# Kernel tuning notes

Hardware: AMD Instinct MI355X
Metric: run time of the kernel (lower is better)

The kernel has to match this reference:

```python
import jax, jax.numpy as jnp
import numpy as np

D_MODEL = 768; D_STATE = 16; D_CONV = 4; EXPAND = 2
D_INNER = EXPAND * D_MODEL          # 1536
DT_RANK = (D_MODEL + 15) // 16      # 48 (mamba_ssm default dt_rank='auto')
BATCH = 2; SEQ = 2048
LN_EPS = 1e-5


def setup_inputs() -> dict:
    key = jax.random.key(0)
    ks = iter(jax.random.split(key, 64))
    def rn(shape, scale=0.02):
        return jax.random.normal(next(ks), shape, jnp.float32) * scale
    inp = {"x": jax.random.normal(next(ks), (BATCH, SEQ, D_MODEL), jnp.float32)}
    for p in ("f", "b"):
        inp[p + "_in_w"]    = rn((2 * D_INNER, D_MODEL))
        inp[p + "_conv_w"]  = rn((D_INNER, D_CONV), 0.2)
        inp[p + "_conv_b"]  = jnp.zeros((D_INNER,), jnp.float32)
        inp[p + "_xproj_w"] = rn((DT_RANK + 2 * D_STATE, D_INNER))
        inp[p + "_dt_w"]    = rn((D_INNER, DT_RANK), 0.1)
        inp[p + "_dt_b"]    = rn((D_INNER,), 0.1)
        inp[p + "_A_log"]   = jnp.log(jnp.broadcast_to(
            jnp.arange(1, D_STATE + 1, dtype=jnp.float32), (D_INNER, D_STATE)))
        inp[p + "_D"]       = jnp.ones((D_INNER,), jnp.float32)
        inp[p + "_out_w"]   = rn((D_MODEL, D_INNER))
    inp["ln1_g"] = jnp.ones((D_MODEL,), jnp.float32)
    inp["ln1_b"] = jnp.zeros((D_MODEL,), jnp.float32)
    inp["ln2_g"] = jnp.ones((D_MODEL,), jnp.float32)
    inp["ln2_b"] = jnp.zeros((D_MODEL,), jnp.float32)
    inp["ff_w1"] = rn((4 * D_MODEL, D_MODEL))
    inp["ff_b1"] = jnp.zeros((4 * D_MODEL,), jnp.float32)
    inp["ff_w2"] = rn((D_MODEL, 4 * D_MODEL))
    inp["ff_b2"] = jnp.zeros((D_MODEL,), jnp.float32)
    return inp


def _layernorm(x, g, b):
    mu = jnp.mean(x, -1, keepdims=True)
    var = jnp.mean((x - mu) ** 2, -1, keepdims=True)
    return (x - mu) * jax.lax.rsqrt(var + LN_EPS) * g + b


def _selective_scan(u, dt, A, Bm, Cm, Dp):
    # u, dt: [B,L,Dh]; A: [Dh,N]; Bm, Cm: [B,L,N]; Dp: [Dh]
    uT, dtT = jnp.swapaxes(u, 0, 1), jnp.swapaxes(dt, 0, 1)   # time-major
    BmT, CmT = jnp.swapaxes(Bm, 0, 1), jnp.swapaxes(Cm, 0, 1)
    h0 = jnp.zeros((u.shape[0], u.shape[2], A.shape[1]), u.dtype)  # [B,Dh,N]
    def step(h, inp):
        u_t, dt_t, b_t, c_t = inp
        dA = jnp.exp(dt_t[:, :, None] * A)                        # [B,Dh,N]
        h = h * dA + (dt_t * u_t)[:, :, None] * b_t[:, None, :]
        return h, jnp.einsum('bdn,bn->bd', h, c_t)
    _, ys = jax.lax.scan(step, h0, (uT, dtT, BmT, CmT))
    return jnp.swapaxes(ys, 0, 1) + u * Dp


def _mamba(x, in_w, conv_w, conv_b, xproj_w, dt_w, dt_b, A_log, Dp, out_w):
    xz = x @ in_w.T                              # [B,L,2*Dh]
    xh, z = jnp.split(xz, 2, axis=-1)
    # causal depthwise conv over time
    xc = jnp.swapaxes(xh, 1, 2)                  # [B,Dh,L]
    xc = jnp.pad(xc, ((0, 0), (0, 0), (D_CONV - 1, 0)))
    xc = jax.lax.conv_general_dilated(xc, conv_w[:, None, :], (1,), 'VALID',
                                      feature_group_count=D_INNER)
    xh = jax.nn.silu(jnp.swapaxes(xc + conv_b[None, :, None], 1, 2))
    x_dbl = xh @ xproj_w.T                       # [B,L,dt_rank+2N]
    dt, Bm, Cm = jnp.split(x_dbl, [DT_RANK, DT_RANK + D_STATE], axis=-1)
    dt = jax.nn.softplus(dt @ dt_w.T + dt_b)     # [B,L,Dh]
    A = -jnp.exp(A_log)                          # [Dh,N]
    y = _selective_scan(xh, dt, A, Bm, Cm, Dp)
    return (y * jax.nn.silu(z)) @ out_w.T


def _forward(x, f_in_w, f_conv_w, f_conv_b, f_xproj_w, f_dt_w, f_dt_b, f_A_log,
             f_D, f_out_w, b_in_w, b_conv_w, b_conv_b, b_xproj_w, b_dt_w, b_dt_b,
             b_A_log, b_D, b_out_w, ln1_g, ln1_b, ln2_g, ln2_b,
             ff_w1, ff_b1, ff_w2, ff_b2):
    xn = _layernorm(x, ln1_g, ln1_b)
    fo = _mamba(xn, f_in_w, f_conv_w, f_conv_b, f_xproj_w, f_dt_w, f_dt_b,
                f_A_log, f_D, f_out_w)
    bo = _mamba(xn[:, ::-1], b_in_w, b_conv_w, b_conv_b, b_xproj_w, b_dt_w,
                b_dt_b, b_A_log, b_D, b_out_w)[:, ::-1]
    m = _layernorm(fo + bo, ln2_g, ln2_b)
    ff = jax.nn.gelu(m @ ff_w1.T + ff_b1, approximate=False) @ ff_w2.T + ff_b2
    return ff + x


def reference(x, f_in_w, f_conv_w, f_conv_b, f_xproj_w, f_dt_w, f_dt_b, f_A_log,
              f_D, f_out_w, b_in_w, b_conv_w, b_conv_b, b_xproj_w, b_dt_w, b_dt_b,
              b_A_log, b_D, b_out_w, ln1_g, ln1_b, ln2_g, ln2_b,
              ff_w1, ff_b1, ff_w2, ff_b2):
    return _forward(x, f_in_w, f_conv_w, f_conv_b, f_xproj_w, f_dt_w, f_dt_b,
                    f_A_log, f_D, f_out_w, b_in_w, b_conv_w, b_conv_b, b_xproj_w,
                    b_dt_w, b_dt_b, b_A_log, b_D, b_out_w, ln1_g, ln1_b, ln2_g,
                    ln2_b, ff_w1, ff_b1, ff_w2, ff_b2)
```

## Files before the change

kernel.cpp:

```cpp
#include <hip/hip_runtime.h>
#include <cstdint>
#include <cstddef>

#define BATCH_ 2
#define SEQ_ 2048
#define DM 768
#define DH 1536
#define NS 16
#define RK 48
#define MR (BATCH_*SEQ_)
#define NCH 32
#define CL (SEQ_/NCH)
#define NCHAN (2*BATCH_*DH)
#define NDBLK (DH/256)

typedef __attribute__((ext_vector_type(8))) short short8b;
typedef __attribute__((ext_vector_type(4))) float f32x4;
typedef __attribute__((address_space(1))) const unsigned int gas_u32;
typedef __attribute__((address_space(3))) unsigned int las_u32;

__device__ __forceinline__ float sigmoidf_(float x){ return 1.f/(1.f+__expf(-x)); }

__device__ __forceinline__ void split1(float x, ushort& h, ushort& l){
  unsigned u = __float_as_uint(x);
  h = (ushort)(u >> 16);
  float lf = x - __uint_as_float(u & 0xFFFF0000u);
  l = (ushort)(__float_as_uint(lf) >> 16);
}

__global__ __launch_bounds__(256) void split_kernel(const float* __restrict__ in,
    ushort* __restrict__ hi, ushort* __restrict__ lo, int n4)
{
  int i = blockIdx.x*256 + threadIdx.x;
  if (i >= n4) return;
  float4 v = ((const float4*)in)[i];
  ushort h0,h1,h2,h3,l0,l1,l2,l3;
  split1(v.x,h0,l0); split1(v.y,h1,l1); split1(v.z,h2,l2); split1(v.w,h3,l3);
  ((ushort4*)hi)[i] = make_ushort4(h0,h1,h2,h3);
  ((ushort4*)lo)[i] = make_ushort4(l0,l1,l2,l3);
}

__global__ __launch_bounds__(256) void ln1_kernel(const float* __restrict__ x,
    const float* __restrict__ g, const float* __restrict__ bta,
    ushort* __restrict__ xnh, ushort* __restrict__ xnl)
{
  int row = blockIdx.x;
  int tid = threadIdx.x;
  __shared__ float s1[256], s2[256];
  float v[3]; float sum=0.f, sq=0.f;
  const float* xr = x + (size_t)row*DM;
  #pragma unroll
  for (int i=0;i<3;i++){ v[i] = xr[tid + i*256]; sum += v[i]; sq += v[i]*v[i]; }
  s1[tid]=sum; s2[tid]=sq; __syncthreads();
  for (int off=128; off>0; off>>=1){
    if (tid<off){ s1[tid]+=s1[tid+off]; s2[tid]+=s2[tid+off]; }
    __syncthreads();
  }
  float mean = s1[0] * (1.f/DM);
  float var  = s2[0] * (1.f/DM) - mean*mean;
  float rstd = rsqrtf(var + 1e-5f);
  #pragma unroll
  for (int i=0;i<3;i++){
    int c = tid + i*256;
    float val = (v[i]-mean)*rstd*g[c] + bta[c];
    ushort h, lo_;
    split1(val, h, lo_);
    xnh[(size_t)row*DM + c] = h;  xnl[(size_t)row*DM + c] = lo_;
  }
}

__global__ __launch_bounds__(256) void ln2_kernel(const float* __restrict__ fo,
    const float* __restrict__ bo, const float* __restrict__ g,
    const float* __restrict__ bta, ushort* __restrict__ mh, ushort* __restrict__ ml)
{
  int row = blockIdx.x;
  int tid = threadIdx.x;
  int bb = row >> 11, l = row & (SEQ_-1);
  __shared__ float s1[256], s2[256];
  size_t rrow = ((size_t)bb*SEQ_ + (SEQ_-1-l))*DM;
  float v[3]; float sum=0.f, sq=0.f;
  #pragma unroll
  for (int i=0;i<3;i++){
    int c = tid + i*256;
    v[i] = fo[(size_t)row*DM + c] + bo[rrow + c];
    sum += v[i]; sq += v[i]*v[i];
  }
  s1[tid]=sum; s2[tid]=sq; __syncthreads();
  for (int off=128; off>0; off>>=1){
    if (tid<off){ s1[tid]+=s1[tid+off]; s2[tid]+=s2[tid+off]; }
    __syncthreads();
  }
  float mean = s1[0] * (1.f/DM);
  float var  = s2[0] * (1.f/DM) - mean*mean;
  float rstd = rsqrtf(var + 1e-5f);
  #pragma unroll
  for (int i=0;i<3;i++){
    int c = tid + i*256;
    float val = (v[i]-mean)*rstd*g[c] + bta[c];
    ushort h, lo_;
    split1(val, h, lo_);
    mh[(size_t)row*DM + c] = h;  ml[(size_t)row*DM + c] = lo_;
  }
}

template<int ACT, bool RAW>
__global__ __launch_bounds__(256) void gemm_nt(const float* __restrict__ A, int lda,
    const float* __restrict__ W, const float* __restrict__ bias,
    float* __restrict__ C, int ldc, const float* __restrict__ res,
    int M, int N, int K, int Kc)
{
  __shared__ float As[16][64];
  __shared__ float Ws[16][64];
  int tid = threadIdx.x;
  int tx = tid & 15, ty = tid >> 4;
  int m0 = blockIdx.y * 64, n0 = blockIdx.x * 64;
  int lm = tid >> 2;
  int lk = (tid & 3) * 4;
  const int kbeg = RAW ? blockIdx.z*Kc : 0;
  const int kend = RAW ? kbeg + Kc : K;
  float acc[4][4] = {};
  for (int k0 = kbeg; k0 < kend; k0 += 16) {
    float4 av = *(const float4*)(A + (size_t)(m0+lm)*lda + k0 + lk);
    As[lk+0][lm] = av.x; As[lk+1][lm] = av.y; As[lk+2][lm] = av.z; As[lk+3][lm] = av.w;
    int wn = n0 + lm;
    float4 wv = make_float4(0.f,0.f,0.f,0.f);
    if (wn < N) wv = *(const float4*)(W + (size_t)wn*K + k0 + lk);
    Ws[lk+0][lm] = wv.x; Ws[lk+1][lm] = wv.y; Ws[lk+2][lm] = wv.z; Ws[lk+3][lm] = wv.w;
    __syncthreads();
    #pragma unroll
    for (int k = 0; k < 16; ++k) {
      float4 a = *(const float4*)&As[k][ty*4];
      float4 w = *(const float4*)&Ws[k][tx*4];
      acc[0][0] += a.x*w.x; acc[0][1] += a.x*w.y; acc[0][2] += a.x*w.z; acc[0][3] += a.x*w.w;
      acc[1][0] += a.y*w.x; acc[1][1] += a.y*w.y; acc[1][2] += a.y*w.z; acc[1][3] += a.y*w.w;
      acc[2][0] += a.z*w.x; acc[2][1] += a.z*w.y; acc[2][2] += a.z*w.z; acc[2][3] += a.z*w.w;
      acc[3][0] += a.w*w.x; acc[3][1] += a.w*w.y; acc[3][2] += a.w*w.z; acc[3][3] += a.w*w.w;
    }
    __syncthreads();
  }
  if constexpr (RAW){
    float* P = C + (size_t)blockIdx.z*((size_t)M*N);
    #pragma unroll
    for (int i=0;i<4;i++){
      int row = m0 + ty*4 + i;
      #pragma unroll
      for (int j=0;j<4;j++){
        int col = n0 + tx*4 + j;
        if (col < N) P[(size_t)row*N + col] = acc[i][j];
      }
    }
  } else {
    #pragma unroll
    for (int i=0;i<4;i++){
      int row = m0 + ty*4 + i;
      #pragma unroll
      for (int j=0;j<4;j++){
        int col = n0 + tx*4 + j;
        if (col < N) {
          float vv = acc[i][j];
          if (bias) vv += bias[col];
          if (ACT == 1) vv = (vv > 20.f) ? vv : log1pf(expf(vv));
          if (res) vv += res[(size_t)row*ldc + col];
          C[(size_t)row*ldc + col] = vv;
        }
      }
    }
  }
}

template<int ACT, int OUT>
__global__ __launch_bounds__(256,2) void gemm_mfma(
    const ushort* __restrict__ Ah_g, const ushort* __restrict__ Al_g, int ldaA,
    const ushort* __restrict__ Wh_g, const ushort* __restrict__ Wl_g,
    const ushort* __restrict__ Wh2, const ushort* __restrict__ Wl2,
    float* __restrict__ C2,
    const float* __restrict__ bias, float* __restrict__ C,
    ushort* __restrict__ Oh, ushort* __restrict__ Ol,
    int ldc, const float* __restrict__ res,
    int M, int N, int K, int Kc)
{
  __shared__ short8b L[2][2048];
  const int tid = threadIdx.x;
  const int m0 = blockIdx.y*128, n0 = blockIdx.x*128;
  const int lane = tid & 63, wv = tid >> 6;
  const int wr = (wv>>1)*64, wc = (wv&1)*64;
  const int li = lane & 15, lg = lane >> 4;
  const int z = blockIdx.z;
  const int kbeg = (OUT==1) ? z*Kc : 0;
  const int nkt = ((OUT==1) ? Kc : K) >> 5;

  const ushort* WhS = Wh_g; const ushort* WlS = Wl_g;
  float* Cd = C;
  int revmask = 0;
  if constexpr (OUT==3){
    if (z==1){ WhS = Wh2; WlS = Wl2; Cd = C2; revmask = SEQ_-1; }
  }

  const int lr8 = lane >> 3, ls = lane & 7;
  const int sl = ls ^ lr8;
  const int chunk = (sl & 3) * 8;
  const ushort* gA = (sl < 4) ? Ah_g : Al_g;
  const ushort* gB = (sl < 4) ? WhS : WlS;
  const ushort* aAddr[4]; const ushort* bAddr[4];
  #pragma unroll
  for (int i=0;i<4;i++){
    int rg = (m0 + wv*32 + i*8 + lr8) ^ revmask;
    aAddr[i] = gA + (size_t)rg*ldaA + kbeg + chunk;
    int rb = n0 + wv*32 + i*8 + lr8;
    bAddr[i] = gB + (size_t)rb*K + kbeg + chunk;
  }

  f32x4 acc[4][4];
  #pragma unroll
  for (int i=0;i<4;i++)
    #pragma unroll
    for (int j=0;j<4;j++) acc[i][j] = (f32x4){0.f,0.f,0.f,0.f};

  #define STAGE_(kt_, b_) { \
    const int ko_ = (kt_)*32; \
    _Pragma("unroll") \
    for (int i=0;i<4;i++){ \
      __builtin_amdgcn_global_load_lds((gas_u32*)(aAddr[i]+ko_), \
          (las_u32*)&L[b_][(wv*32+i*8)*8], 16, 0, 0); \
      __builtin_amdgcn_global_load_lds((gas_u32*)(bAddr[i]+ko_), \
          (las_u32*)&L[b_][1024+(wv*32+i*8)*8], 16, 0, 0); \
    } }

  STAGE_(0, 0);
  __syncthreads();

  for (int kt=0; kt<nkt; ++kt){
    const int cur = kt & 1;
    if (kt+1 < nkt) STAGE_(kt+1, cur^1);
    short8b afh[4],afl[4],bfh[4],bfl[4];
    #pragma unroll
    for (int f=0; f<4; f++){
      int sa = (wr+f*16+li)*8 + (lg ^ (li&7));
      int sb = 1024 + (wc+f*16+li)*8 + (lg ^ (li&7));
      afh[f]=L[cur][sa]; afl[f]=L[cur][sa^4];
      bfh[f]=L[cur][sb]; bfl[f]=L[cur][sb^4];
    }
    #pragma unroll
    for (int fr=0;fr<4;fr++)
      #pragma unroll
      for (int fc=0;fc<4;fc++){
        acc[fr][fc]=__builtin_amdgcn_mfma_f32_16x16x32_bf16(afh[fr],bfh[fc],acc[fr][fc],0,0,0);
        acc[fr][fc]=__builtin_amdgcn_mfma_f32_16x16x32_bf16(afh[fr],bfl[fc],acc[fr][fc],0,0,0);
        acc[fr][fc]=__builtin_amdgcn_mfma_f32_16x16x32_bf16(afl[fr],bfh[fc],acc[fr][fc],0,0,0);
      }
    __syncthreads();
  }
  #undef STAGE_

  if constexpr (OUT==1){
    float* P = C + (size_t)z*((size_t)M*N);
    #pragma unroll
    for (int fr=0;fr<4;fr++)
      #pragma unroll
      for (int fc=0;fc<4;fc++){
        int col = n0 + wc + fc*16 + li;
        int row = m0 + wr + fr*16 + lg*4;
        #pragma unroll
        for (int rg=0;rg<4;rg++)
          P[(size_t)(row+rg)*N + col] = acc[fr][fc][rg];
      }
  } else if constexpr (OUT==2){
    #pragma unroll
    for (int fr=0;fr<4;fr++)
      #pragma unroll
      for (int fc=0;fc<4;fc++){
        int col = n0 + wc + fc*16 + li;
        int row = m0 + wr + fr*16 + lg*4;
        float bv = bias ? bias[col] : 0.f;
        #pragma unroll
        for (int rg=0;rg<4;rg++){
          float t = acc[fr][fc][rg] + bv;
          t = 0.5f*t*(1.f+erff(t*0.70710678118654752f));
          ushort h, lo_;
          split1(t, h, lo_);
          Oh[(size_t)(row+rg)*ldc + col] = h;
          Ol[(size_t)(row+rg)*ldc + col] = lo_;
        }
      }
  } else {
    #pragma unroll
    for (int fr=0;fr<4;fr++)
      #pragma unroll
      for (int fc=0;fc<4;fc++){
        int col = n0 + wc + fc*16 + li;
        int row = m0 + wr + fr*16 + lg*4;
        float bv = bias ? bias[col] : 0.f;
        #pragma unroll
        for (int rg=0;rg<4;rg++){
          float t = acc[fr][fc][rg] + bv;
          if (res) t += res[(size_t)(row+rg)*ldc + col];
          Cd[(size_t)(row+rg)*ldc + col] = t;
        }
      }
  }
}

__global__ __launch_bounds__(256) void reduce_split(const float* __restrict__ P,
    const float* __restrict__ bias, const float* __restrict__ res,
    float* __restrict__ C, int N, size_t elems, int nsplit)
{
  size_t i = ((size_t)blockIdx.x*256 + threadIdx.x)*4;
  float4 s = *(const float4*)(P + i);
  for (int k=1;k<nsplit;k++){
    float4 p = *(const float4*)(P + (size_t)k*elems + i);
    s.x+=p.x; s.y+=p.y; s.z+=p.z; s.w+=p.w;
  }
  if (bias){
    int col = (int)(i % (size_t)N);
    const float4 b = *(const float4*)(bias + col);
    s.x+=b.x; s.y+=b.y; s.z+=b.z; s.w+=b.w;
  }
  if (res){
    const float4 r = *(const float4*)(res + i);
    s.x+=r.x; s.y+=r.y; s.z+=r.z; s.w+=r.w;
  }
  *(float4*)(C + i) = s;
}

__global__ __launch_bounds__(256) void conv_silu_kernel(const float* __restrict__ xz,
    const float* __restrict__ cw, const float* __restrict__ cb, float* __restrict__ xh)
{
  int idx = blockIdx.x*256 + threadIdx.x;
  int d = idx % DH;
  int row = idx / DH;
  int l = row & (SEQ_-1);
  const float* base = xz + (size_t)row*(2*DH) + d;
  float acc = cb[d];
  #pragma unroll
  for (int j=0;j<4;j++){
    int ll = l - 3 + j;
    if (ll >= 0) acc += cw[d*4+j] * base[(ptrdiff_t)(j-3)*(2*DH)];
  }
  xh[(size_t)row*DH + d] = acc * sigmoidf_(acc);
}

__global__ __launch_bounds__(256) void scan_p1_kernel(
    const float* __restrict__ dt0, const float* __restrict__ xh0, const float* __restrict__ xd0,
    const float* __restrict__ Al0,
    const float* __restrict__ dt1, const float* __restrict__ xh1, const float* __restrict__ xd1,
    const float* __restrict__ Al1,
    float* __restrict__ hend, float* __restrict__ dtsum)
{
  int tid = threadIdx.x;
  int bid = blockIdx.x;
  int dblk = bid % NDBLK;
  int t   = bid / NDBLK;
  int c   = t & (NCH-1);
  int db  = t >> 5;
  int dir = db >> 1, bb = db & 1;
  int d = dblk*256 + tid;
  const float* dt = dir ? dt1 : dt0;
  const float* xh = dir ? xh1 : xh0;
  const float* xd = dir ? xd1 : xd0;
  const float* Al = dir ? Al1 : Al0;

  __shared__ float sB[CL][NS];
  {
    const float* xdb = xd + ((size_t)bb*SEQ_ + (size_t)c*CL)*80 + RK;
    int row = tid >> 2, part = tid & 3;
    *(float4*)&sB[row][part*4] = *(const float4*)(xdb + (size_t)row*80 + part*4);
  }
  float An[NS];
  {
    const float4* ap = (const float4*)(Al + (size_t)d*NS);
    #pragma unroll
    for (int q=0;q<4;q++){
      float4 a = ap[q];
      An[4*q+0] = -__expf(a.x); An[4*q+1] = -__expf(a.y);
      An[4*q+2] = -__expf(a.z); An[4*q+3] = -__expf(a.w);
    }
  }
  __syncthreads();

  float h[NS];
  #pragma unroll
  for (int n=0;n<NS;n++) h[n] = 0.f;
  float dts = 0.f;
  size_t base = ((size_t)bb*SEQ_ + (size_t)c*CL)*DH + d;
  #pragma unroll 4
  for (int l=0;l<CL;++l){
    float dtv = dt[base], uv = xh[base];
    float du = dtv*uv;
    float Bv[NS];
    *(float4*)&Bv[0]  = *(const float4*)&sB[l][0];
    *(float4*)&Bv[4]  = *(const float4*)&sB[l][4];
    *(float4*)&Bv[8]  = *(const float4*)&sB[l][8];
    *(float4*)&Bv[12] = *(const float4*)&sB[l][12];
    #pragma unroll
    for (int n=0;n<NS;n++)
      h[n] = h[n]*__expf(dtv*An[n]) + du*Bv[n];
    dts += dtv;
    base += DH;
  }
  size_t unit = ((size_t)db*DH + d)*NCH + c;
  float4* hp = (float4*)(hend + unit*NS);
  hp[0] = make_float4(h[0],h[1],h[2],h[3]);
  hp[1] = make_float4(h[4],h[5],h[6],h[7]);
  hp[2] = make_float4(h[8],h[9],h[10],h[11]);
  hp[3] = make_float4(h[12],h[13],h[14],h[15]);
  dtsum[(size_t)c*NCHAN + (size_t)db*DH + d] = dts;
}

__global__ __launch_bounds__(256) void scan_p2_kernel(
    const float* __restrict__ Al0, const float* __restrict__ Al1,
    float* __restrict__ hend, const float* __restrict__ dtsum)
{
  int t = blockIdx.x*256 + threadIdx.x;
  int n = t & 15;
  int ch = t >> 4;
  int d  = ch % DH;
  int dir = (ch / DH) >> 1;
  const float* Al = dir ? Al1 : Al0;
  float An = -__expf(Al[d*NS + n]);
  float h0 = 0.f;
  size_t ub = (size_t)ch * NCH;
  #pragma unroll
  for (int c = 0; c < NCH; ++c) {
    float P  = __expf(An * dtsum[(size_t)c*NCHAN + ch]);
    float he = hend[(ub + c)*NS + n];
    hend[(ub + c)*NS + n] = h0;
    h0 = h0 * P + he;
  }
}

__global__ __launch_bounds__(256) void scan_p3_kernel(
    const float* __restrict__ dt0, const float* __restrict__ xh0, const float* __restrict__ xd0,
    const float* __restrict__ z0, const float* __restrict__ Al0, const float* __restrict__ Dp0,
    ushort* __restrict__ yg0,
    const float* __restrict__ dt1, const float* __restrict__ xh1, const float* __restrict__ xd1,
    const float* __restrict__ z1, const float* __restrict__ Al1, const float* __restrict__ Dp1,
    ushort* __restrict__ yg1,
    const float* __restrict__ hstart)
{
  int tid = threadIdx.x;
  int bid = blockIdx.x;
  int dblk = bid % NDBLK;
  int t   = bid / NDBLK;
  int c   = t & (NCH-1);
  int db  = t >> 5;
  int dir = db >> 1, bb = db & 1;
  int d = dblk*256 + tid;
  const float* dt = dir ? dt1 : dt0;
  const float* xh = dir ? xh1 : xh0;
  const float* xd = dir ? xd1 : xd0;
  const float* zp = dir ? z1  : z0;
  const float* Al = dir ? Al1 : Al0;
  const float* Dp = dir ? Dp1 : Dp0;
  ushort*      yg = dir ? yg1 : yg0;

  __shared__ float sBC[CL][2*NS];
  {
    const float* xdb = xd + ((size_t)bb*SEQ_ + (size_t)c*CL)*80 + RK;
    #pragma unroll
    for (int i=0;i<2;i++){
      int idx = tid + i*256;
      int row = idx >> 3, part = idx & 7;
      *(float4*)&sBC[row][part*4] = *(const float4*)(xdb + (size_t)row*80 + part*4);
    }
  }
  float An[NS];
  {
    const float4* ap = (const float4*)(Al + (size_t)d*NS);
    #pragma unroll
    for (int q=0;q<4;q++){
      float4 a = ap[q];
      An[4*q+0] = -__expf(a.x); An[4*q+1] = -__expf(a.y);
      An[4*q+2] = -__expf(a.z); An[4*q+3] = -__expf(a.w);
    }
  }
  float Dd = Dp[d];
  __syncthreads();

  size_t unit = ((size_t)db*DH + d)*NCH + c;
  float h[NS];
  {
    const float4* hp = (const float4*)(hstart + unit*NS);
    float4 h0=hp[0], h1=hp[1], h2=hp[2], h3=hp[3];
    h[0]=h0.x; h[1]=h0.y; h[2]=h0.z; h[3]=h0.w;
    h[4]=h1.x; h[5]=h1.y; h[6]=h1.z; h[7]=h1.w;
    h[8]=h2.x; h[9]=h2.y; h[10]=h2.z; h[11]=h2.w;
    h[12]=h3.x; h[13]=h3.y; h[14]=h3.z; h[15]=h3.w;
  }
  size_t base = ((size_t)bb*SEQ_ + (size_t)c*CL)*DH + d;
  size_t zidx = ((size_t)bb*SEQ_ + (size_t)c*CL)*(size_t)(2*DH) + DH + d;
  size_t yrow = ((size_t)bb*SEQ_ + (size_t)c*CL)*(size_t)(4*DH) + d;
  #pragma unroll 2
  for (int l=0;l<CL;++l){
    float dtv = dt[base], uv = xh[base];
    float zv = zp[zidx];
    float du = dtv*uv;
    float Bv[NS], Cv[NS];
    *(float4*)&Bv[0]  = *(const float4*)&sBC[l][0];
    *(float4*)&Bv[4]  = *(const float4*)&sBC[l][4];
    *(float4*)&Bv[8]  = *(const float4*)&sBC[l][8];
    *(float4*)&Bv[12] = *(const float4*)&sBC[l][12];
    *(float4*)&Cv[0]  = *(const float4*)&sBC[l][16];
    *(float4*)&Cv[4]  = *(const float4*)&sBC[l][20];
    *(float4*)&Cv[8]  = *(const float4*)&sBC[l][24];
    *(float4*)&Cv[12] = *(const float4*)&sBC[l][28];
    float y = 0.f;
    #pragma unroll
    for (int n=0;n<NS;n++){
      h[n] = h[n]*__expf(dtv*An[n]) + du*Bv[n];
      y = fmaf(h[n], Cv[n], y);
    }
    float yv = (y + uv*Dd) * (zv * sigmoidf_(zv));
    ushort hh, ll;
    split1(yv, hh, ll);
    yg[yrow] = hh; yg[yrow + DH] = ll;
    base += DH; zidx += 2*DH; yrow += 4*DH;
  }
}

template<int ACT>
static inline void launch_gemm(const float* A, int lda, const float* W, const float* bias,
                               float* C, int ldc, const float* res,
                               int M, int N, int K, hipStream_t s)
{
  dim3 grid((N+63)/64, M/64);
  gemm_nt<ACT,false><<<grid, dim3(256), 0, s>>>(A, lda, W, bias, C, ldc, res, M, N, K, 0);
}

static inline void launch_gemm_splitk(const float* A, int lda, const float* W,
                                      float* P, int M, int N, int K, int nsplit,
                                      hipStream_t s)
{
  dim3 grid((N+63)/64, M/64, nsplit);
  gemm_nt<0,true><<<grid, dim3(256), 0, s>>>(A, lda, W, nullptr, P, N, nullptr,
                                             M, N, K, K/nsplit);
}

extern "C" void kernel_launch(void* const* d_in, const int* in_sizes, int n_in,
                              void* d_out, int out_size, void* d_ws, size_t ws_size,
                              hipStream_t stream)
{
  const float* x        = (const float*)d_in[0];
  const float* f_in_w   = (const float*)d_in[1];
  const float* f_conv_w = (const float*)d_in[2];
  const float* f_conv_b = (const float*)d_in[3];
  const float* f_xproj  = (const float*)d_in[4];
  const float* f_dt_w   = (const float*)d_in[5];
  const float* f_dt_b   = (const float*)d_in[6];
  const float* f_A_log  = (const float*)d_in[7];
  const float* f_D      = (const float*)d_in[8];
  const float* f_out_w  = (const float*)d_in[9];
  const float* b_in_w   = (const float*)d_in[10];
  const float* b_conv_w = (const float*)d_in[11];
  const float* b_conv_b = (const float*)d_in[12];
  const float* b_xproj  = (const float*)d_in[13];
  const float* b_dt_w   = (const float*)d_in[14];
  const float* b_dt_b   = (const float*)d_in[15];
  const float* b_A_log  = (const float*)d_in[16];
  const float* b_D      = (const float*)d_in[17];
  const float* b_out_w  = (const float*)d_in[18];
  const float* ln1_g    = (const float*)d_in[19];
  const float* ln1_b    = (const float*)d_in[20];
  const float* ln2_g    = (const float*)d_in[21];
  const float* ln2_b    = (const float*)d_in[22];
  const float* ff_w1    = (const float*)d_in[23];
  const float* ff_b1    = (const float*)d_in[24];
  const float* ff_w2    = (const float*)d_in[25];
  const float* ff_b2    = (const float*)d_in[26];
  float* out = (float*)d_out;

  float* ws = (float*)d_ws;
  size_t o = 0;
  float* xz_f   = ws + o; o += (size_t)MR*2*DH;
  float* xz_b   = ws + o; o += (size_t)MR*2*DH;
  float* xh_f   = ws + o; o += (size_t)MR*DH;
  float* xh_b   = ws + o; o += (size_t)MR*DH;
  float* xdbl_f = ws + o; o += (size_t)MR*80;
  float* xdbl_b = ws + o; o += (size_t)MR*80;
  float* dtb_f  = ws + o; o += (size_t)MR*DH;
  float* dtb_b  = ws + o; o += (size_t)MR*DH;
  float* xnbf   = ws + o; o += (size_t)MR*DM;
  float* dtsum  = ws + o; o += (size_t)NCHAN*NCH;
  float* wbf    = ws + o; o += (size_t)2*(2*DH*DM);

  ushort* xnh = (ushort*)xnbf;
  ushort* xnl = xnh + (size_t)MR*DM;
  ushort* yg_f = (ushort*)xz_f;
  ushort* yg_b = (ushort*)xz_b;
  ushort* wreg = (ushort*)wbf;
  ushort* f_inh = wreg;                       ushort* f_inl = wreg + (size_t)2*DH*DM;
  ushort* b_inh = wreg + (size_t)2*(2*DH*DM); ushort* b_inl = wreg + (size_t)3*(2*DH*DM);
  ushort* f_oth = wreg;                       ushort* f_otl = wreg + (size_t)DM*DH;
  ushort* b_oth = wreg + (size_t)2*DM*DH;     ushort* b_otl = wreg + (size_t)3*DM*DH;
  ushort* w1h   = wreg;                       ushort* w1l   = wreg + (size_t)4*DM*DM;
  ushort* w2h   = wreg + (size_t)2*(4*DM*DM); ushort* w2l   = wreg + (size_t)3*(4*DM*DM);
  float* hend  = xnbf;
  float* partX = xnbf;
  ushort* mh   = (ushort*)xh_f;
  ushort* ml   = mh + (size_t)MR*DM;
  float* fo    = xh_b;
  float* bo    = xh_b + (size_t)MR*DM;
  float* part1 = dtb_f;
  ushort* ffhh = (ushort*)dtb_f;
  ushort* ffhl = ffhh + (size_t)MR*4*DM;
  float* part2 = xz_b;
  const size_t EL = (size_t)MR*DM;
  const size_t EL2 = (size_t)MR*80;

  split_kernel<<<(2*DH*DM/4+255)/256, 256, 0, stream>>>(f_in_w, f_inh, f_inl, 2*DH*DM/4);
  split_kernel<<<(2*DH*DM/4+255)/256, 256, 0, stream>>>(b_in_w, b_inh, b_inl, 2*DH*DM/4);
  ln1_kernel<<<MR, 256, 0, stream>>>(x, ln1_g, ln1_b, xnh, xnl);
  {
    dim3 grid((2*DH)/128, MR/128, 2);
    gemm_mfma<0,3><<<grid, dim3(256), 0, stream>>>(xnh, xnl, DM, f_inh, f_inl,
        b_inh, b_inl, xz_b, nullptr, xz_f, nullptr, nullptr, 2*DH, nullptr,
        MR, 2*DH, DM, 0);
  }
  split_kernel<<<(DM*DH/4+255)/256, 256, 0, stream>>>(f_out_w, f_oth, f_otl, DM*DH/4);
  split_kernel<<<(DM*DH/4+255)/256, 256, 0, stream>>>(b_out_w, b_oth, b_otl, DM*DH/4);
  conv_silu_kernel<<<(MR*DH)/256, 256, 0, stream>>>(xz_f, f_conv_w, f_conv_b, xh_f);
  conv_silu_kernel<<<(MR*DH)/256, 256, 0, stream>>>(xz_b, b_conv_w, b_conv_b, xh_b);
  launch_gemm_splitk(xh_f, DH, f_xproj, partX, MR, 80, DH, 8, stream);
  reduce_split<<<(int)(EL2/1024), 256, 0, stream>>>(partX, nullptr, nullptr, xdbl_f, 80, EL2, 8);
  launch_gemm_splitk(xh_b, DH, b_xproj, partX, MR, 80, DH, 8, stream);
  reduce_split<<<(int)(EL2/1024), 256, 0, stream>>>(partX, nullptr, nullptr, xdbl_b, 80, EL2, 8);
  launch_gemm<1>(xdbl_f, 80, f_dt_w, f_dt_b, dtb_f, DH, nullptr, MR, DH, RK, stream);
  launch_gemm<1>(xdbl_b, 80, b_dt_w, b_dt_b, dtb_b, DH, nullptr, MR, DH, RK, stream);
  scan_p1_kernel<<<4*NCH*NDBLK, 256, 0, stream>>>(
      dtb_f, xh_f, xdbl_f, f_A_log,
      dtb_b, xh_b, xdbl_b, b_A_log,
      hend, dtsum);
  scan_p2_kernel<<<(NCHAN*NS)/256, 256, 0, stream>>>(f_A_log, b_A_log, hend, dtsum);
  scan_p3_kernel<<<4*NCH*NDBLK, 256, 0, stream>>>(
      dtb_f, xh_f, xdbl_f, xz_f, f_A_log, f_D, yg_f,
      dtb_b, xh_b, xdbl_b, xz_b, b_A_log, b_D, yg_b,
      hend);
  {
    dim3 grid(DM/128, MR/128, 4);
    gemm_mfma<0,1><<<grid, dim3(256), 0, stream>>>(yg_f, yg_f + DH, 4*DH,
        f_oth, f_otl, nullptr, nullptr, nullptr, nullptr, part1, nullptr, nullptr,
        DM, nullptr, MR, DM, DH, DH/4);
    reduce_split<<<(int)(EL/1024), 256, 0, stream>>>(part1, nullptr, nullptr, fo, DM, EL, 4);
    gemm_mfma<0,1><<<grid, dim3(256), 0, stream>>>(yg_b, yg_b + DH, 4*DH,
        b_oth, b_otl, nullptr, nullptr, nullptr, nullptr, part1, nullptr, nullptr,
        DM, nullptr, MR, DM, DH, DH/4);
    reduce_split<<<(int)(EL/1024), 256, 0, stream>>>(part1, nullptr, nullptr, bo, DM, EL, 4);
  }
  split_kernel<<<(4*DM*DM/4+255)/256, 256, 0, stream>>>(ff_w1, w1h, w1l, 4*DM*DM/4);
  split_kernel<<<(4*DM*DM/4+255)/256, 256, 0, stream>>>(ff_w2, w2h, w2l, 4*DM*DM/4);
  ln2_kernel<<<MR, 256, 0, stream>>>(fo, bo, ln2_g, ln2_b, mh, ml);
  {
    dim3 grid1((4*DM)/128, MR/128);
    gemm_mfma<2,2><<<grid1, dim3(256), 0, stream>>>(mh, ml, DM, w1h, w1l,
        nullptr, nullptr, nullptr, ff_b1, nullptr, ffhh, ffhl, 4*DM, nullptr,
        MR, 4*DM, DM, 0);
    dim3 grid2(DM/128, MR/128, 4);
    gemm_mfma<0,1><<<grid2, dim3(256), 0, stream>>>(ffhh, ffhl, 4*DM, w2h, w2l,
        nullptr, nullptr, nullptr, nullptr, part2, nullptr, nullptr,
        DM, nullptr, MR, DM, 4*DM, (4*DM)/4);
    reduce_split<<<(int)(EL/1024), 256, 0, stream>>>(part2, ff_b2, x, out, DM, EL, 4);
  }
}
```

Measured before the change: 779.0 us.

## Move x_proj and dt_proj GEMMs to split-bf16 MFMA path with padded weights

```diff
diff --git a/kernel.cpp b/kernel.cpp
--- a/kernel.cpp
+++ b/kernel.cpp
@@ -8,6 +8,8 @@
 #define DH 1536
 #define NS 16
 #define RK 48
+#define XDW 128
+#define KDT 64
 #define MR (BATCH_*SEQ_)
 #define NCH 32
 #define CL (SEQ_/NCH)
@@ -26,6 +28,9 @@
   h = (ushort)(u >> 16);
   float lf = x - __uint_as_float(u & 0xFFFF0000u);
   l = (ushort)(__float_as_uint(lf) >> 16);
+}
+__device__ __forceinline__ float joinhl(ushort h, ushort l){
+  return __uint_as_float((unsigned)h<<16) + __uint_as_float((unsigned)l<<16);
 }
 
 __global__ __launch_bounds__(256) void split_kernel(const float* __restrict__ in,
@@ -40,6 +45,19 @@
   ((ushort4*)lo)[i] = make_ushort4(l0,l1,l2,l3);
 }
 
+__global__ __launch_bounds__(256) void padsplit_kernel(const float* __restrict__ in,
+    ushort* __restrict__ hi, ushort* __restrict__ lo,
+    int rin, int cin, int rout, int cout)
+{
+  int i = blockIdx.x*256 + threadIdx.x;
+  if (i >= rout*cout) return;
+  int r = i / cout, c = i % cout;
+  float v = (r < rin && c < cin) ? in[(size_t)r*cin + c] : 0.f;
+  ushort h, l;
+  split1(v, h, l);
+  hi[i] = h; lo[i] = l;
+}
+
 __global__ __launch_bounds__(256) void ln1_kernel(const float* __restrict__ x,
     const float* __restrict__ g, const float* __restrict__ bta,
     ushort* __restrict__ xnh, ushort* __restrict__ xnl)
@@ -100,71 +118,6 @@
     ushort h, lo_;
     split1(val, h, lo_);
     mh[(size_t)row*DM + c] = h;  ml[(size_t)row*DM + c] = lo_;
-  }
-}
-
-template<int ACT, bool RAW>
-__global__ __launch_bounds__(256) void gemm_nt(const float* __restrict__ A, int lda,
-    const float* __restrict__ W, const float* __restrict__ bias,
-    float* __restrict__ C, int ldc, const float* __restrict__ res,
-    int M, int N, int K, int Kc)
-{
-  __shared__ float As[16][64];
-  __shared__ float Ws[16][64];
-  int tid = threadIdx.x;
-  int tx = tid & 15, ty = tid >> 4;
-  int m0 = blockIdx.y * 64, n0 = blockIdx.x * 64;
-  int lm = tid >> 2;
-  int lk = (tid & 3) * 4;
-  const int kbeg = RAW ? blockIdx.z*Kc : 0;
-  const int kend = RAW ? kbeg + Kc : K;
-  float acc[4][4] = {};
-  for (int k0 = kbeg; k0 < kend; k0 += 16) {
-    float4 av = *(const float4*)(A + (size_t)(m0+lm)*lda + k0 + lk);
-    As[lk+0][lm] = av.x; As[lk+1][lm] = av.y; As[lk+2][lm] = av.z; As[lk+3][lm] = av.w;
-    int wn = n0 + lm;
-    float4 wv = make_float4(0.f,0.f,0.f,0.f);
-    if (wn < N) wv = *(const float4*)(W + (size_t)wn*K + k0 + lk);
-    Ws[lk+0][lm] = wv.x; Ws[lk+1][lm] = wv.y; Ws[lk+2][lm] = wv.z; Ws[lk+3][lm] = wv.w;
-    __syncthreads();
-    #pragma unroll
-    for (int k = 0; k < 16; ++k) {
-      float4 a = *(const float4*)&As[k][ty*4];
-      float4 w = *(const float4*)&Ws[k][tx*4];
-      acc[0][0] += a.x*w.x; acc[0][1] += a.x*w.y; acc[0][2] += a.x*w.z; acc[0][3] += a.x*w.w;
-      acc[1][0] += a.y*w.x; acc[1][1] += a.y*w.y; acc[1][2] += a.y*w.z; acc[1][3] += a.y*w.w;
-      acc[2][0] += a.z*w.x; acc[2][1] += a.z*w.y; acc[2][2] += a.z*w.z; acc[2][3] += a.z*w.w;
-      acc[3][0] += a.w*w.x; acc[3][1] += a.w*w.y; acc[3][2] += a.w*w.z; acc[3][3] += a.w*w.w;
-    }
-    __syncthreads();
-  }
-  if constexpr (RAW){
-    float* P = C + (size_t)blockIdx.z*((size_t)M*N);
-    #pragma unroll
-    for (int i=0;i<4;i++){
-      int row = m0 + ty*4 + i;
-      #pragma unroll
-      for (int j=0;j<4;j++){
-        int col = n0 + tx*4 + j;
-        if (col < N) P[(size_t)row*N + col] = acc[i][j];
-      }
-    }
-  } else {
-    #pragma unroll
-    for (int i=0;i<4;i++){
-      int row = m0 + ty*4 + i;
-      #pragma unroll
-      for (int j=0;j<4;j++){
-        int col = n0 + tx*4 + j;
-        if (col < N) {
-          float vv = acc[i][j];
-          if (bias) vv += bias[col];
-          if (ACT == 1) vv = (vv > 20.f) ? vv : log1pf(expf(vv));
-          if (res) vv += res[(size_t)row*ldc + col];
-          C[(size_t)row*ldc + col] = vv;
-        }
-      }
-    }
   }
 }
 
@@ -181,11 +134,22 @@
 {
   __shared__ short8b L[2][2048];
   const int tid = threadIdx.x;
-  const int m0 = blockIdx.y*128, n0 = blockIdx.x*128;
+  int bx = blockIdx.x, by = blockIdx.y, bz = blockIdx.z;
+  {
+    const int Gx = gridDim.x, Gy = gridDim.y;
+    const int n = Gx*Gy*gridDim.z;
+    if ((n & 7) == 0){
+      int lid = bx + Gx*(by + Gy*bz);
+      int lid2 = (lid & 7)*(n >> 3) + (lid >> 3);
+      bx = lid2 % Gx; lid2 /= Gx;
+      by = lid2 % Gy; bz = lid2 / Gy;
+    }
+  }
+  const int m0 = by*128, n0 = bx*128;
   const int lane = tid & 63, wv = tid >> 6;
   const int wr = (wv>>1)*64, wc = (wv&1)*64;
   const int li = lane & 15, lg = lane >> 4;
-  const int z = blockIdx.z;
+  const int z = bz;
   const int kbeg = (OUT==1) ? z*Kc : 0;
   const int nkt = ((OUT==1) ? Kc : K) >> 5;
 
@@ -293,6 +257,7 @@
         #pragma unroll
         for (int rg=0;rg<4;rg++){
           float t = acc[fr][fc][rg] + bv;
+          if constexpr (ACT==1) t = (t > 20.f) ? t : log1pf(expf(t));
           if (res) t += res[(size_t)(row+rg)*ldc + col];
           Cd[(size_t)(row+rg)*ldc + col] = t;
         }
@@ -322,8 +287,35 @@
   *(float4*)(C + i) = s;
 }
 
+__global__ __launch_bounds__(256) void reduce_xproj(const float* __restrict__ P,
+    float* __restrict__ xdbl, ushort* __restrict__ aH, ushort* __restrict__ aL,
+    size_t elems, int nsplit)
+{
+  size_t i = ((size_t)blockIdx.x*256 + threadIdx.x)*4;
+  float4 s = *(const float4*)(P + i);
+  for (int k=1;k<nsplit;k++){
+    float4 p = *(const float4*)(P + (size_t)k*elems + i);
+    s.x+=p.x; s.y+=p.y; s.z+=p.z; s.w+=p.w;
+  }
+  *(float4*)(xdbl + i) = s;
+  int col = (int)(i & (XDW-1));
+  if (col < KDT){
+    size_t row = i >> 7;
+    float vs[4] = {s.x, s.y, s.z, s.w};
+    ushort h[4], l[4];
+    #pragma unroll
+    for (int j=0;j<4;j++){
+      float v = (col + j < RK) ? vs[j] : 0.f;
+      split1(v, h[j], l[j]);
+    }
+    *(ushort4*)(aH + row*KDT + col) = make_ushort4(h[0],h[1],h[2],h[3]);
+    *(ushort4*)(aL + row*KDT + col) = make_ushort4(l[0],l[1],l[2],l[3]);
+  }
+}
+
 __global__ __launch_bounds__(256) void conv_silu_kernel(const float* __restrict__ xz,
-    const float* __restrict__ cw, const float* __restrict__ cb, float* __restrict__ xh)
+    const float* __restrict__ cw, const float* __restrict__ cb,
+    ushort* __restrict__ xhh, ushort* __restrict__ xhl)
 {
   int idx = blockIdx.x*256 + threadIdx.x;
   int d = idx % DH;
@@ -336,13 +328,18 @@
     int ll = l - 3 + j;
     if (ll >= 0) acc += cw[d*4+j] * base[(ptrdiff_t)(j-3)*(2*DH)];
   }
-  xh[(size_t)row*DH + d] = acc * sigmoidf_(acc);
+  float v = acc * sigmoidf_(acc);
+  ushort h, lo_;
+  split1(v, h, lo_);
+  xhh[idx] = h; xhl[idx] = lo_;
 }
 
 __global__ __launch_bounds__(256) void scan_p1_kernel(
-    const float* __restrict__ dt0, const float* __restrict__ xh0, const float* __restrict__ xd0,
+    const float* __restrict__ dt0, const ushort* __restrict__ xhh0,
+    const ushort* __restrict__ xhl0, const float* __restrict__ xd0,
     const float* __restrict__ Al0,
-    const float* __restrict__ dt1, const float* __restrict__ xh1, const float* __restrict__ xd1,
+    const float* __restrict__ dt1, const ushort* __restrict__ xhh1,
+    const ushort* __restrict__ xhl1, const float* __restrict__ xd1,
     const float* __restrict__ Al1,
     float* __restrict__ hend, float* __restrict__ dtsum)
 {
@@ -355,15 +352,16 @@
   int dir = db >> 1, bb = db & 1;
   int d = dblk*256 + tid;
   const float* dt = dir ? dt1 : dt0;
-  const float* xh = dir ? xh1 : xh0;
+  const ushort* xhh = dir ? xhh1 : xhh0;
+  const ushort* xhl = dir ? xhl1 : xhl0;
   const float* xd = dir ? xd1 : xd0;
   const float* Al = dir ? Al1 : Al0;
 
   __shared__ float sB[CL][NS];
   {
-    const float* xdb = xd + ((size_t)bb*SEQ_ + (size_t)c*CL)*80 + RK;
+    const float* xdb = xd + ((size_t)bb*SEQ_ + (size_t)c*CL)*XDW + RK;
     int row = tid >> 2, part = tid & 3;
-    *(float4*)&sB[row][part*4] = *(const float4*)(xdb + (size_t)row*80 + part*4);
+    *(float4*)&sB[row][part*4] = *(const float4*)(xdb + (size_t)row*XDW + part*4);
   }
   float An[NS];
   {
@@ -384,7 +382,8 @@
   size_t base = ((size_t)bb*SEQ_ + (size_t)c*CL)*DH + d;
   #pragma unroll 4
   for (int l=0;l<CL;++l){
-    float dtv = dt[base], uv = xh[base];
+    float dtv = dt[base];
+    float uv = joinhl(xhh[base], xhl[base]);
     float du = dtv*uv;
     float Bv[NS];
     *(float4*)&Bv[0]  = *(const float4*)&sB[l][0];
@@ -429,12 +428,14 @@
 }
 
 __global__ __launch_bounds__(256) void scan_p3_kernel(
-    const float* __restrict__ dt0, const float* __restrict__ xh0, const float* __restrict__ xd0,
-    const float* __restrict__ z0, const float* __restrict__ Al0, const float* __restrict__ Dp0,
-    ushort* __restrict__ yg0,
-    const float* __restrict__ dt1, const float* __restrict__ xh1, const float* __restrict__ xd1,
-    const float* __restrict__ z1, const float* __restrict__ Al1, const float* __restrict__ Dp1,
-    ushort* __restrict__ yg1,
+    const float* __restrict__ dt0, const ushort* __restrict__ xhh0,
+    const ushort* __restrict__ xhl0, const float* __restrict__ xd0,
+    const float* __restrict__ z0, const float* __restrict__ Al0,
+    const float* __restrict__ Dp0, ushort* __restrict__ yg0,
+    const float* __restrict__ dt1, const ushort* __restrict__ xhh1,
+    const ushort* __restrict__ xhl1, const float* __restrict__ xd1,
+    const float* __restrict__ z1, const float* __restrict__ Al1,
+    const float* __restrict__ Dp1, ushort* __restrict__ yg1,
     const float* __restrict__ hstart)
 {
   int tid = threadIdx.x;
@@ -446,7 +447,8 @@
   int dir = db >> 1, bb = db & 1;
   int d = dblk*256 + tid;
   const float* dt = dir ? dt1 : dt0;
-  const float* xh = dir ? xh1 : xh0;
+  const ushort* xhh = dir ? xhh1 : xhh0;
+  const ushort* xhl = dir ? xhl1 : xhl0;
   const float* xd = dir ? xd1 : xd0;
   const float* zp = dir ? z1  : z0;
   const float* Al = dir ? Al1 : Al0;
@@ -455,12 +457,12 @@
 
   __shared__ float sBC[CL][2*NS];
   {
-    const float* xdb = xd + ((size_t)bb*SEQ_ + (size_t)c*CL)*80 + RK;
+    const float* xdb = xd + ((size_t)bb*SEQ_ + (size_t)c*CL)*XDW + RK;
     #pragma unroll
     for (int i=0;i<2;i++){
       int idx = tid + i*256;
       int row = idx >> 3, part = idx & 7;
-      *(float4*)&sBC[row][part*4] = *(const float4*)(xdb + (size_t)row*80 + part*4);
+      *(float4*)&sBC[row][part*4] = *(const float4*)(xdb + (size_t)row*XDW + part*4);
     }
   }
   float An[NS];
@@ -491,7 +493,8 @@
   size_t yrow = ((size_t)bb*SEQ_ + (size_t)c*CL)*(size_t)(4*DH) + d;
   #pragma unroll 2
   for (int l=0;l<CL;++l){
-    float dtv = dt[base], uv = xh[base];
+    float dtv = dt[base];
+    float uv = joinhl(xhh[base], xhl[base]);
     float zv = zp[zidx];
     float du = dtv*uv;
     float Bv[NS], Cv[NS];
@@ -515,24 +518,6 @@
     yg[yrow] = hh; yg[yrow + DH] = ll;
     base += DH; zidx += 2*DH; yrow += 4*DH;
   }
-}
-
-template<int ACT>
-static inline void launch_gemm(const float* A, int lda, const float* W, const float* bias,
-                               float* C, int ldc, const float* res,
-                               int M, int N, int K, hipStream_t s)
-{
-  dim3 grid((N+63)/64, M/64);
-  gemm_nt<ACT,false><<<grid, dim3(256), 0, s>>>(A, lda, W, bias, C, ldc, res, M, N, K, 0);
-}
-
-static inline void launch_gemm_splitk(const float* A, int lda, const float* W,
-                                      float* P, int M, int N, int K, int nsplit,
-                                      hipStream_t s)
-{
-  dim3 grid((N+63)/64, M/64, nsplit);
-  gemm_nt<0,true><<<grid, dim3(256), 0, s>>>(A, lda, W, nullptr, P, N, nullptr,
-                                             M, N, K, K/nsplit);
 }
 
 extern "C" void kernel_launch(void* const* d_in, const int* in_sizes, int n_in,
@@ -574,16 +559,23 @@
   float* xz_b   = ws + o; o += (size_t)MR*2*DH;
   float* xh_f   = ws + o; o += (size_t)MR*DH;
   float* xh_b   = ws + o; o += (size_t)MR*DH;
-  float* xdbl_f = ws + o; o += (size_t)MR*80;
-  float* xdbl_b = ws + o; o += (size_t)MR*80;
+  float* xdbl_f = ws + o; o += (size_t)MR*XDW;
+  float* xdbl_b = ws + o; o += (size_t)MR*XDW;
   float* dtb_f  = ws + o; o += (size_t)MR*DH;
   float* dtb_b  = ws + o; o += (size_t)MR*DH;
+  float* dthA_f = ws + o; o += (size_t)MR*KDT;
+  float* dthA_b = ws + o; o += (size_t)MR*KDT;
   float* xnbf   = ws + o; o += (size_t)MR*DM;
   float* dtsum  = ws + o; o += (size_t)NCHAN*NCH;
   float* wbf    = ws + o; o += (size_t)2*(2*DH*DM);
+  float* wsm    = ws + o; o += (size_t)2*128*DH + (size_t)2*DH*KDT;
 
   ushort* xnh = (ushort*)xnbf;
   ushort* xnl = xnh + (size_t)MR*DM;
+  ushort* xhh_f = (ushort*)xh_f;  ushort* xhl_f = xhh_f + (size_t)MR*DH;
+  ushort* xhh_b = (ushort*)xh_b;  ushort* xhl_b = xhh_b + (size_t)MR*DH;
+  ushort* aHf = (ushort*)dthA_f;  ushort* aLf = aHf + (size_t)MR*KDT;
+  ushort* aHb = (ushort*)dthA_b;  ushort* aLb = aHb + (size_t)MR*KDT;
   ushort* yg_f = (ushort*)xz_f;
   ushort* yg_b = (ushort*)xz_b;
   ushort* wreg = (ushort*)wbf;
@@ -593,8 +585,13 @@
   ushort* b_oth = wreg + (size_t)2*DM*DH;     ushort* b_otl = wreg + (size_t)3*DM*DH;
   ushort* w1h   = wreg;                       ushort* w1l   = wreg + (size_t)4*DM*DM;
   ushort* w2h   = wreg + (size_t)2*(4*DM*DM); ushort* w2l   = wreg + (size_t)3*(4*DM*DM);
+  ushort* wsu = (ushort*)wsm;
+  ushort* xpwh_f = wsu;                         ushort* xpwl_f = xpwh_f + (size_t)128*DH;
+  ushort* xpwh_b = xpwl_f + (size_t)128*DH;     ushort* xpwl_b = xpwh_b + (size_t)128*DH;
+  ushort* dtwh_f = xpwl_b + (size_t)128*DH;     ushort* dtwl_f = dtwh_f + (size_t)DH*KDT;
+  ushort* dtwh_b = dtwl_f + (size_t)DH*KDT;     ushort* dtwl_b = dtwh_b + (size_t)DH*KDT;
   float* hend  = xnbf;
-  float* partX = xnbf;
+  float* partX = dtb_f;
   ushort* mh   = (ushort*)xh_f;
   ushort* ml   = mh + (size_t)MR*DM;
   float* fo    = xh_b;
@@ -603,11 +600,15 @@
   ushort* ffhh = (ushort*)dtb_f;
   ushort* ffhl = ffhh + (size_t)MR*4*DM;
   float* part2 = xz_b;
-  const size_t EL = (size_t)MR*DM;
-  const size_t EL2 = (size_t)MR*80;
+  const size_t EL  = (size_t)MR*DM;
+  const size_t ELX = (size_t)MR*XDW;
 
   split_kernel<<<(2*DH*DM/4+255)/256, 256, 0, stream>>>(f_in_w, f_inh, f_inl, 2*DH*DM/4);
   split_kernel<<<(2*DH*DM/4+255)/256, 256, 0, stream>>>(b_in_w, b_inh, b_inl, 2*DH*DM/4);
+  padsplit_kernel<<<(128*DH+255)/256, 256, 0, stream>>>(f_xproj, xpwh_f, xpwl_f, 80, DH, 128, DH);
+  padsplit_kernel<<<(128*DH+255)/256, 256, 0, stream>>>(b_xproj, xpwh_b, xpwl_b, 80, DH, 128, DH);
+  padsplit_kernel<<<(DH*KDT+255)/256, 256, 0, stream>>>(f_dt_w, dtwh_f, dtwl_f, DH, RK, DH, KDT);
+  padsplit_kernel<<<(DH*KDT+255)/256, 256, 0, stream>>>(b_dt_w, dtwh_b, dtwl_b, DH, RK, DH, KDT);
   ln1_kernel<<<MR, 256, 0, stream>>>(x, ln1_g, ln1_b, xnh, xnl);
   {
     dim3 grid((2*DH)/128, MR/128, 2);
@@ -617,22 +618,36 @@
   }
   split_kernel<<<(DM*DH/4+255)/256, 256, 0, stream>>>(f_out_w, f_oth, f_otl, DM*DH/4);
   split_kernel<<<(DM*DH/4+255)/256, 256, 0, stream>>>(b_out_w, b_oth, b_otl, DM*DH/4);
-  conv_silu_kernel<<<(MR*DH)/256, 256, 0, stream>>>(xz_f, f_conv_w, f_conv_b, xh_f);
-  conv_silu_kernel<<<(MR*DH)/256, 256, 0, stream>>>(xz_b, b_conv_w, b_conv_b, xh_b);
-  launch_gemm_splitk(xh_f, DH, f_xproj, partX, MR, 80, DH, 8, stream);
-  reduce_split<<<(int)(EL2/1024), 256, 0, stream>>>(partX, nullptr, nullptr, xdbl_f, 80, EL2, 8);
-  launch_gemm_splitk(xh_b, DH, b_xproj, partX, MR, 80, DH, 8, stream);
-  reduce_split<<<(int)(EL2/1024), 256, 0, stream>>>(partX, nullptr, nullptr, xdbl_b, 80, EL2, 8);
-  launch_gemm<1>(xdbl_f, 80, f_dt_w, f_dt_b, dtb_f, DH, nullptr, MR, DH, RK, stream);
-  launch_gemm<1>(xdbl_b, 80, b_dt_w, b_dt_b, dtb_b, DH, nullptr, MR, DH, RK, stream);
+  conv_silu_kernel<<<(MR*DH)/256, 256, 0, stream>>>(xz_f, f_conv_w, f_conv_b, xhh_f, xhl_f);
+  conv_silu_kernel<<<(MR*DH)/256, 256, 0, stream>>>(xz_b, b_conv_w, b_conv_b, xhh_b, xhl_b);
+  {
+    dim3 grid(1, MR/128, 8);
+    gemm_mfma<0,1><<<grid, dim3(256), 0, stream>>>(xhh_f, xhl_f, DH, xpwh_f, xpwl_f,
+        nullptr, nullptr, nullptr, nullptr, partX, nullptr, nullptr,
+        XDW, nullptr, MR, XDW, DH, DH/8);
+    reduce_xproj<<<(int)(ELX/1024), 256, 0, stream>>>(partX, xdbl_f, aHf, aLf, ELX, 8);
+    gemm_mfma<0,1><<<grid, dim3(256), 0, stream>>>(xhh_b, xhl_b, DH, xpwh_b, xpwl_b,
+        nullptr, nullptr, nullptr, nullptr, partX, nullptr, nullptr,
+        XDW, nullptr, MR, XDW, DH, DH/8);
+    reduce_xproj<<<(int)(ELX/1024), 256, 0, stream>>>(partX, xdbl_b, aHb, aLb, ELX, 8);
+  }
+  {
+    dim3 grid(DH/128, MR/128, 1);
+    gemm_mfma<1,0><<<grid, dim3(256), 0, stream>>>(aHf, aLf, KDT, dtwh_f, dtwl_f,
+        nullptr, nullptr, nullptr, f_dt_b, dtb_f, nullptr, nullptr,
+        DH, nullptr, MR, DH, KDT, 0);
+    gemm_mfma<1,0><<<grid, dim3(256), 0, stream>>>(aHb, aLb, KDT, dtwh_b, dtwl_b,
+        nullptr, nullptr, nullptr, b_dt_b, dtb_b, nullptr, nullptr,
+        DH, nullptr, MR, DH, KDT, 0);
+  }
   scan_p1_kernel<<<4*NCH*NDBLK, 256, 0, stream>>>(
-      dtb_f, xh_f, xdbl_f, f_A_log,
-      dtb_b, xh_b, xdbl_b, b_A_log,
+      dtb_f, xhh_f, xhl_f, xdbl_f, f_A_log,
+      dtb_b, xhh_b, xhl_b, xdbl_b, b_A_log,
       hend, dtsum);
   scan_p2_kernel<<<(NCHAN*NS)/256, 256, 0, stream>>>(f_A_log, b_A_log, hend, dtsum);
   scan_p3_kernel<<<4*NCH*NDBLK, 256, 0, stream>>>(
-      dtb_f, xh_f, xdbl_f, xz_f, f_A_log, f_D, yg_f,
-      dtb_b, xh_b, xdbl_b, xz_b, b_A_log, b_D, yg_b,
+      dtb_f, xhh_f, xhl_f, xdbl_f, xz_f, f_A_log, f_D, yg_f,
+      dtb_b, xhh_b, xhl_b, xdbl_b, xz_b, b_A_log, b_D, yg_b,
       hend);
   {
     dim3 grid(DM/128, MR/128, 4);
@@ -649,7 +664,7 @@
   split_kernel<<<(4*DM*DM/4+255)/256, 256, 0, stream>>>(ff_w2, w2h, w2l, 4*DM*DM/4);
   ln2_kernel<<<MR, 256, 0, stream>>>(fo, bo, ln2_g, ln2_b, mh, ml);
   {
-    dim3 grid1((4*DM)/128, MR/128);
+    dim3 grid1((4*DM)/128, MR/128, 1);
     gemm_mfma<2,2><<<grid1, dim3(256), 0, stream>>>(mh, ml, DM, w1h, w1l,
         nullptr, nullptr, nullptr, ff_b1, nullptr, ffhh, ffhl, 4*DM, nullptr,
         MR, 4*DM, DM, 0);
```

After: 873.6 us. +12.1%, slower.

## Add single-buffer GEMM variant and XCD-aware block remapping

Applied to the files above, without the earlier changes.

```diff
diff --git a/kernel.cpp b/kernel.cpp
--- a/kernel.cpp
+++ b/kernel.cpp
@@ -168,7 +168,7 @@
   }
 }
 
-template<int ACT, int OUT>
+template<int ACT, int OUT, bool PIPE2>
 __global__ __launch_bounds__(256,2) void gemm_mfma(
     const ushort* __restrict__ Ah_g, const ushort* __restrict__ Al_g, int ldaA,
     const ushort* __restrict__ Wh_g, const ushort* __restrict__ Wl_g,
@@ -179,13 +179,24 @@
     int ldc, const float* __restrict__ res,
     int M, int N, int K, int Kc)
 {
-  __shared__ short8b L[2][2048];
+  __shared__ short8b L[(PIPE2?2:1)*2048];
   const int tid = threadIdx.x;
-  const int m0 = blockIdx.y*128, n0 = blockIdx.x*128;
+  int bx = blockIdx.x, by = blockIdx.y, bz = blockIdx.z;
+  {
+    const int Gx = gridDim.x, Gy = gridDim.y;
+    const int n = Gx*Gy*gridDim.z;
+    if ((n & 7) == 0){
+      int lid = bx + Gx*(by + Gy*bz);
+      int lid2 = (lid & 7)*(n >> 3) + (lid >> 3);
+      bx = lid2 % Gx; lid2 /= Gx;
+      by = lid2 % Gy; bz = lid2 / Gy;
+    }
+  }
+  const int m0 = by*128, n0 = bx*128;
   const int lane = tid & 63, wv = tid >> 6;
   const int wr = (wv>>1)*64, wc = (wv&1)*64;
   const int li = lane & 15, lg = lane >> 4;
-  const int z = blockIdx.z;
+  const int z = bz;
   const int kbeg = (OUT==1) ? z*Kc : 0;
   const int nkt = ((OUT==1) ? Kc : K) >> 5;
 
@@ -221,36 +232,48 @@
     _Pragma("unroll") \
     for (int i=0;i<4;i++){ \
       __builtin_amdgcn_global_load_lds((gas_u32*)(aAddr[i]+ko_), \
-          (las_u32*)&L[b_][(wv*32+i*8)*8], 16, 0, 0); \
+          (las_u32*)&L[(b_)*2048 + (wv*32+i*8)*8], 16, 0, 0); \
       __builtin_amdgcn_global_load_lds((gas_u32*)(bAddr[i]+ko_), \
-          (las_u32*)&L[b_][1024+(wv*32+i*8)*8], 16, 0, 0); \
+          (las_u32*)&L[(b_)*2048 + 1024 + (wv*32+i*8)*8], 16, 0, 0); \
     } }
 
-  STAGE_(0, 0);
-  __syncthreads();
-
-  for (int kt=0; kt<nkt; ++kt){
-    const int cur = kt & 1;
-    if (kt+1 < nkt) STAGE_(kt+1, cur^1);
-    short8b afh[4],afl[4],bfh[4],bfl[4];
-    #pragma unroll
-    for (int f=0; f<4; f++){
-      int sa = (wr+f*16+li)*8 + (lg ^ (li&7));
-      int sb = 1024 + (wc+f*16+li)*8 + (lg ^ (li&7));
-      afh[f]=L[cur][sa]; afl[f]=L[cur][sa^4];
-      bfh[f]=L[cur][sb]; bfl[f]=L[cur][sb^4];
-    }
-    #pragma unroll
-    for (int fr=0;fr<4;fr++)
-      #pragma unroll
-      for (int fc=0;fc<4;fc++){
-        acc[fr][fc]=__builtin_amdgcn_mfma_f32_16x16x32_bf16(afh[fr],bfh[fc],acc[fr][fc],0,0,0);
-        acc[fr][fc]=__builtin_amdgcn_mfma_f32_16x16x32_bf16(afh[fr],bfl[fc],acc[fr][fc],0,0,0);
-        acc[fr][fc]=__builtin_amdgcn_mfma_f32_16x16x32_bf16(afl[fr],bfh[fc],acc[fr][fc],0,0,0);
-      }
+  #define COMPUTE_(base_) { \
+    short8b afh[4],afl[4],bfh[4],bfl[4]; \
+    _Pragma("unroll") \
+    for (int f=0; f<4; f++){ \
+      int sa = (base_) + (wr+f*16+li)*8 + (lg ^ (li&7)); \
+      int sb = (base_) + 1024 + (wc+f*16+li)*8 + (lg ^ (li&7)); \
+      afh[f]=L[sa]; afl[f]=L[sa^4]; \
+      bfh[f]=L[sb]; bfl[f]=L[sb^4]; \
+    } \
+    _Pragma("unroll") \
+    for (int fr=0;fr<4;fr++) \
+      _Pragma("unroll") \
+      for (int fc=0;fc<4;fc++){ \
+        acc[fr][fc]=__builtin_amdgcn_mfma_f32_16x16x32_bf16(afh[fr],bfh[fc],acc[fr][fc],0,0,0); \
+        acc[fr][fc]=__builtin_amdgcn_mfma_f32_16x16x32_bf16(afh[fr],bfl[fc],acc[fr][fc],0,0,0); \
+        acc[fr][fc]=__builtin_amdgcn_mfma_f32_16x16x32_bf16(afl[fr],bfh[fc],acc[fr][fc],0,0,0); \
+      } }
+
+  if constexpr (PIPE2){
+    STAGE_(0, 0);
     __syncthreads();
+    for (int kt=0; kt<nkt; ++kt){
+      const int cur = kt & 1;
+      if (kt+1 < nkt) STAGE_(kt+1, cur^1);
+      COMPUTE_(cur*2048);
+      __syncthreads();
+    }
+  } else {
+    for (int kt=0; kt<nkt; ++kt){
+      STAGE_(kt, 0);
+      __syncthreads();
+      COMPUTE_(0);
+      __syncthreads();
+    }
   }
   #undef STAGE_
+  #undef COMPUTE_
 
   if constexpr (OUT==1){
     float* P = C + (size_t)z*((size_t)M*N);
@@ -611,7 +634,7 @@
   ln1_kernel<<<MR, 256, 0, stream>>>(x, ln1_g, ln1_b, xnh, xnl);
   {
     dim3 grid((2*DH)/128, MR/128, 2);
-    gemm_mfma<0,3><<<grid, dim3(256), 0, stream>>>(xnh, xnl, DM, f_inh, f_inl,
+    gemm_mfma<0,3,true><<<grid, dim3(256), 0, stream>>>(xnh, xnl, DM, f_inh, f_inl,
         b_inh, b_inl, xz_b, nullptr, xz_f, nullptr, nullptr, 2*DH, nullptr,
         MR, 2*DH, DM, 0);
   }
@@ -636,11 +659,11 @@
       hend);
   {
     dim3 grid(DM/128, MR/128, 4);
-    gemm_mfma<0,1><<<grid, dim3(256), 0, stream>>>(yg_f, yg_f + DH, 4*DH,
+    gemm_mfma<0,1,false><<<grid, dim3(256), 0, stream>>>(yg_f, yg_f + DH, 4*DH,
         f_oth, f_otl, nullptr, nullptr, nullptr, nullptr, part1, nullptr, nullptr,
         DM, nullptr, MR, DM, DH, DH/4);
     reduce_split<<<(int)(EL/1024), 256, 0, stream>>>(part1, nullptr, nullptr, fo, DM, EL, 4);
-    gemm_mfma<0,1><<<grid, dim3(256), 0, stream>>>(yg_b, yg_b + DH, 4*DH,
+    gemm_mfma<0,1,false><<<grid, dim3(256), 0, stream>>>(yg_b, yg_b + DH, 4*DH,
         b_oth, b_otl, nullptr, nullptr, nullptr, nullptr, part1, nullptr, nullptr,
         DM, nullptr, MR, DM, DH, DH/4);
     reduce_split<<<(int)(EL/1024), 256, 0, stream>>>(part1, nullptr, nullptr, bo, DM, EL, 4);
@@ -649,12 +672,12 @@
   split_kernel<<<(4*DM*DM/4+255)/256, 256, 0, stream>>>(ff_w2, w2h, w2l, 4*DM*DM/4);
   ln2_kernel<<<MR, 256, 0, stream>>>(fo, bo, ln2_g, ln2_b, mh, ml);
   {
-    dim3 grid1((4*DM)/128, MR/128);
-    gemm_mfma<2,2><<<grid1, dim3(256), 0, stream>>>(mh, ml, DM, w1h, w1l,
+    dim3 grid1((4*DM)/128, MR/128, 1);
+    gemm_mfma<2,2,false><<<grid1, dim3(256), 0, stream>>>(mh, ml, DM, w1h, w1l,
         nullptr, nullptr, nullptr, ff_b1, nullptr, ffhh, ffhl, 4*DM, nullptr,
         MR, 4*DM, DM, 0);
     dim3 grid2(DM/128, MR/128, 4);
-    gemm_mfma<0,1><<<grid2, dim3(256), 0, stream>>>(ffhh, ffhl, 4*DM, w2h, w2l,
+    gemm_mfma<0,1,false><<<grid2, dim3(256), 0, stream>>>(ffhh, ffhl, 4*DM, w2h, w2l,
         nullptr, nullptr, nullptr, nullptr, part2, nullptr, nullptr,
         DM, nullptr, MR, DM, 4*DM, (4*DM)/4);
     reduce_split<<<(int)(EL/1024), 256, 0, stream>>>(part2, ff_b2, x, out, DM, EL, 4);
```

Result: faster. 719.0 us (-7.7%).
